# Kernel tuning notes

Hardware: AMD Instinct MI355X
Metric: run time of the kernel (lower is better)

## Reference

```python
import jax, jax.numpy as jnp
import numpy as np

N_NODES = 100000
N_EDGES = 1600000
IN_DIM = 128
HID_DIM = 128
OUT_DIM = 64
BN_EPS = 1e-5


def setup_inputs() -> dict:
    key = jax.random.key(0)
    ks = jax.random.split(key, 8)
    x = jax.random.normal(ks[0], (N_NODES, IN_DIM), dtype=jnp.float32)
    edge_index = jax.random.randint(ks[1], (2, N_EDGES), 0, N_NODES, dtype=jnp.int64)
    s1 = 1.0 / np.sqrt(IN_DIM)
    s2 = 1.0 / np.sqrt(HID_DIM)
    return {
        "x": x,
        "edge_index": edge_index,
        "W1l": jax.random.normal(ks[2], (HID_DIM, IN_DIM), dtype=jnp.float32) * s1,
        "b1l": jnp.zeros((HID_DIM,), dtype=jnp.float32),
        "W1r": jax.random.normal(ks[3], (HID_DIM, IN_DIM), dtype=jnp.float32) * s1,
        "bn_gamma": jnp.ones((HID_DIM,), dtype=jnp.float32),
        "bn_beta": jnp.zeros((HID_DIM,), dtype=jnp.float32),
        "bn_mean": jnp.zeros((HID_DIM,), dtype=jnp.float32),
        "bn_var": jnp.ones((HID_DIM,), dtype=jnp.float32),
        "W2l": jax.random.normal(ks[4], (OUT_DIM, HID_DIM), dtype=jnp.float32) * s2,
        "b2l": jnp.zeros((OUT_DIM,), dtype=jnp.float32),
        "W2r": jax.random.normal(ks[5], (OUT_DIM, HID_DIM), dtype=jnp.float32) * s2,
    }


def _sage_conv(x, src, dst, Wl, bl, Wr, num_nodes):
    # message = x[src], mean-aggregated at dst; out = lin_l(agg) + lin_r(x)
    msgs = x[src]  # [E, D] gather (memory bound)
    agg = jax.ops.segment_sum(msgs, dst, num_segments=num_nodes)
    deg = jax.ops.segment_sum(jnp.ones((src.shape[0],), dtype=x.dtype), dst,
                              num_segments=num_nodes)
    agg = agg / jnp.maximum(deg, 1.0)[:, None]
    return agg @ Wl.T + bl + x @ Wr.T


def reference(x, edge_index, W1l, b1l, W1r, bn_gamma, bn_beta, bn_mean, bn_var,
              W2l, b2l, W2r):
    src, dst = edge_index[0], edge_index[1]
    n = x.shape[0]
    h = _sage_conv(x, src, dst, W1l, b1l, W1r, n)
    # BatchNorm1d (inference: running stats), then ReLU; dropout is identity in eval
    h = (h - bn_mean) * (bn_gamma * jax.lax.rsqrt(bn_var + BN_EPS)) + bn_beta
    h = jax.nn.relu(h)
    return _sage_conv(h, src, dst, W2l, b2l, W2r, n)
```

## Files before the change

kernel.cpp:

```cpp
#include <hip/hip_runtime.h>
#include <hip/hip_fp16.h>

#define N_NODES 100000
#define N_EDGES 1600000
#define TILE 2048
#define NBUK 64
#define BSH 11
#define NBUK_USED ((N_NODES + (1 << BSH) - 1) >> BSH)
#define CAP 36864
#define SMASK 0x1FFFF

typedef _Float16 f16x8 __attribute__((ext_vector_type(8)));
typedef float    f32x4 __attribute__((ext_vector_type(4)));

__global__ __launch_bounds__(256) void k_pre(
    const float* __restrict__ x, __half* __restrict__ x_h,
    const float* __restrict__ W1l, const float* __restrict__ W1r,
    const float* __restrict__ W2l, const float* __restrict__ W2r,
    __half* __restrict__ W1lf, __half* __restrict__ W1rf,
    __half* __restrict__ W2f, int* __restrict__ bcur)
{
    int i = blockIdx.x * 256 + threadIdx.x;
    if (i < N_NODES * 32) {
        float4 v = ((const float4*)x)[i];
        __half2 a = __floats2half2_rn(v.x, v.y);
        __half2 b = __floats2half2_rn(v.z, v.w);
        uint2 u = make_uint2(*(unsigned*)&a, *(unsigned*)&b);
        ((uint2*)x_h)[i] = u;
    }
    if (i < 49152) {
        int tt = i & 16383;
        int j    = tt & 7;
        int lane = (tt >> 3) & 63;
        int ks   = (tt >> 9) & 3;
        int ct   = tt >> 11;
        int m = lane & 15, q = lane >> 4;
        int row = ct * 16 + m;
        int col = ks * 32 + q * 8 + j;
        if (i < 16384) {
            W1lf[tt] = __float2half(W1l[row * 128 + col]);
        } else if (i < 32768) {
            W1rf[tt] = __float2half(W1r[row * 128 + col]);
        } else {
            float v = (ct < 4) ? W2l[row * 128 + col]
                               : W2r[(row - 64) * 128 + col];
            W2f[tt] = __float2half(v);
        }
    }
    if (i < NBUK) bcur[i] = i * CAP;
}

__global__ __launch_bounds__(256) void k_binA(
    const int* __restrict__ ei, int* __restrict__ bcur,
    int2* __restrict__ ebuf)
{
    __shared__ int2 scratch[TILE];
    __shared__ int hist[NBUK];
    __shared__ int tstart[NBUK];
    __shared__ int gbase[NBUK];
    int t = threadIdx.x;
    int e0 = blockIdx.x * TILE;
    int tile_n = min(TILE, N_EDGES - e0);
    if (t < NBUK) hist[t] = 0;
    __syncthreads();
    int srcs[8], dsts[8], rank[8], bks[8];
    #pragma unroll
    for (int i = 0; i < 8; ++i) {
        int e = e0 + i * 256 + t;
        bks[i] = -1;
        if (e < N_EDGES) {
            srcs[i] = ei[e];
            dsts[i] = ei[N_EDGES + e];
            bks[i]  = (dsts[i] >> BSH) & (NBUK - 1);
            rank[i] = atomicAdd(&hist[bks[i]], 1);
        }
    }
    __syncthreads();
    if (t == 0) {
        int s = 0;
        #pragma unroll
        for (int b = 0; b < NBUK; ++b) { tstart[b] = s; s += hist[b]; }
    }
    __syncthreads();
    if (t < NBUK && hist[t] > 0)
        gbase[t] = atomicAdd(&bcur[t], hist[t]);
    __syncthreads();
    #pragma unroll
    for (int i = 0; i < 8; ++i)
        if (bks[i] >= 0) {
            int sl = tstart[bks[i]] + rank[i];
            scratch[min(sl, TILE - 1)] = make_int2(srcs[i], dsts[i]);
        }
    __syncthreads();
    for (int p = t; p < tile_n; p += 256) {
        int2 sd = scratch[p];
        int b = (sd.y >> BSH) & (NBUK - 1);
        int o = gbase[b] + (p - tstart[b]);
        ebuf[min(max(o, 0), NBUK * CAP - 1)] = sd;
    }
}

__global__ __launch_bounds__(1024) void k_fillC2(
    const int2* __restrict__ ebuf, const int* __restrict__ bcur,
    int* __restrict__ row_ptr, int* __restrict__ csr_src)
{
    __shared__ int hist[1 << BSH];
    __shared__ int psum[1024];
    __shared__ int cur[1 << BSH];
    __shared__ int bb_l[NBUK_USED + 1];
    int t = threadIdx.x;
    int b = blockIdx.x;
    int base = b << BSH;
    hist[t] = 0;
    hist[t + 1024] = 0;
    if (t < 64) {
        int c = (t < NBUK_USED) ? (bcur[t] - t * CAP) : 0;
        c = min(max(c, 0), CAP);
        int s = c;
        #pragma unroll
        for (int off = 1; off < 64; off <<= 1) {
            int v = __shfl_up(s, off);
            if (t >= off) s += v;
        }
        if (t < NBUK_USED) bb_l[t] = s - c;
        if (t == NBUK_USED - 1) bb_l[NBUK_USED] = s;
    }
    __syncthreads();
    int bb  = bb_l[b];
    int cnt = min(bb_l[b + 1] - bb, CAP);
    const int2* eb = ebuf + (size_t)b * CAP;
    for (int p = t; p < cnt; p += 1024)
        atomicAdd(&hist[(eb[p].y - base) & ((1 << BSH) - 1)], 1);
    __syncthreads();
    int h0 = hist[2 * t], h1 = hist[2 * t + 1];
    psum[t] = h0 + h1;
    __syncthreads();
    #pragma unroll
    for (int off = 1; off < 1024; off <<= 1) {
        int v = (t >= off) ? psum[t - off] : 0;
        __syncthreads();
        psum[t] += v;
        __syncthreads();
    }
    int e0 = bb + psum[t] - (h0 + h1);
    int e1 = e0 + h0;
    int n0g = base + 2 * t, n1g = n0g + 1;
    if (n0g <= N_NODES) row_ptr[n0g] = e0;
    if (n1g <= N_NODES) row_ptr[n1g] = e1;
    cur[2 * t]     = e0;
    cur[2 * t + 1] = e1;
    __syncthreads();
    for (int p = t; p < cnt; p += 1024) {
        int2 sd = eb[p];
        int pos = atomicAdd(&cur[(sd.y - base) & ((1 << BSH) - 1)], 1);
        csr_src[min(max(pos, 0), N_EDGES - 1)] = sd.x;
    }
}

__device__ __forceinline__ void acc_row8(
    const __half* __restrict__ x_h, int s, int col, float4& acc)
{
    uint2 u = ((const uint2*)(x_h + (size_t)(s & SMASK) * 128))[col];
    __half2 a = *(__half2*)&u.x;
    __half2 b = *(__half2*)&u.y;
    float2 fa = __half22float2(a);
    float2 fb = __half22float2(b);
    acc.x += fa.x; acc.y += fa.y; acc.z += fb.x; acc.w += fb.y;
}

__global__ __launch_bounds__(256) void k_agg1(
    const int* __restrict__ row_ptr, const int* __restrict__ csr_src,
    const __half* __restrict__ x_h, __half* __restrict__ agg_h)
{
    int tid  = threadIdx.x;
    int lane = tid & 63;
    int half = lane >> 5;
    int col  = lane & 31;
    int n    = blockIdx.x * 4 + (tid >> 6);
    int e1 = min(row_ptr[n + 1], N_EDGES);
    int e0 = min(max(row_ptr[n], 0), e1);
    float4 acc = make_float4(0.f, 0.f, 0.f, 0.f);
    for (int eb = e0; eb < e1; eb += 64) {
        int cnt = min(e1 - eb, 64);
        int sv = csr_src[min(eb + lane, N_EDGES - 1)];
        int j = 0;
        for (; j + 8 <= cnt; j += 8) {
            #pragma unroll
            for (int u = 0; u < 4; ++u) {
                int sa = __builtin_amdgcn_readlane(sv, j + 2 * u);
                int sb = __builtin_amdgcn_readlane(sv, j + 2 * u + 1);
                int s  = half ? sb : sa;
                acc_row8(x_h, s, col, acc);
            }
        }
        for (; j + 2 <= cnt; j += 2) {
            int sa = __builtin_amdgcn_readlane(sv, j);
            int sb = __builtin_amdgcn_readlane(sv, j + 1);
            int s  = half ? sb : sa;
            acc_row8(x_h, s, col, acc);
        }
        if (j < cnt) {
            int sa = __builtin_amdgcn_readlane(sv, j);
            if (half == 0) acc_row8(x_h, sa, col, acc);
        }
    }
    acc.x += __shfl_xor(acc.x, 32);
    acc.y += __shfl_xor(acc.y, 32);
    acc.z += __shfl_xor(acc.z, 32);
    acc.w += __shfl_xor(acc.w, 32);
    if (half == 0) {
        __half2 h0 = __floats2half2_rn(acc.x, acc.y);
        __half2 h1 = __floats2half2_rn(acc.z, acc.w);
        uint2 u = make_uint2(*(unsigned*)&h0, *(unsigned*)&h1);
        ((uint2*)agg_h)[n * 32 + col] = u;
    }
}

__global__ __launch_bounds__(256) void k_g12(
    const __half* __restrict__ agg_h, const int* __restrict__ row_ptr,
    const __half* __restrict__ x_h,
    const __half* __restrict__ W1lf, const float* __restrict__ b1l,
    const __half* __restrict__ W1rf,
    const float* __restrict__ gamma, const float* __restrict__ beta,
    const float* __restrict__ mean, const float* __restrict__ var,
    const __half* __restrict__ W2f, const float* __restrict__ b2l,
    __half* __restrict__ p2, float* __restrict__ out)
{
    __shared__ char sm[34816];
    __half (*Aagg)[64][8] = (__half(*)[64][8])sm;
    __half (*Ax)[64][8]   = (__half(*)[64][8])(sm + 16384);
    __half (*Ah)[64][8]   = (__half(*)[64][8])sm;
    float  (*Cs)[132]     = (float(*)[132])sm;
    int tid = threadIdx.x;
    int n0  = blockIdx.x * 64;

    {
        int n  = tid & 63;
        int kg = tid >> 6;
        int ng = n0 + n;
        const uint4* pa = (const uint4*)(agg_h + (size_t)ng * 128 + kg * 32);
        const uint4* px = (const uint4*)(x_h   + (size_t)ng * 128 + kg * 32);
        #pragma unroll
        for (int i = 0; i < 4; ++i) {
            uint4 va = make_uint4(0, 0, 0, 0), vx = va;
            if (ng < N_NODES) { va = pa[i]; vx = px[i]; }
            *(uint4*)&Aagg[kg * 4 + i][n][0] = va;
            *(uint4*)&Ax[kg * 4 + i][n][0]   = vx;
        }
    }
    __syncthreads();

    int lane = tid & 63;
    int w = tid >> 6;
    int m = lane & 15;
    int q = lane >> 4;
    int row = w * 16 + m;
    const __half* bl0 = W1lf + (lane << 3);
    const __half* br0 = W1rf + (lane << 3);
    f32x4 accL[8], accR[8];
    #pragma unroll
    for (int c = 0; c < 8; ++c) {
        accL[c] = (f32x4){0.f, 0.f, 0.f, 0.f};
        accR[c] = (f32x4){0.f, 0.f, 0.f, 0.f};
    }
    #pragma unroll
    for (int ks = 0; ks < 4; ++ks) {
        f16x8 aL = *(const f16x8*)&Aagg[ks * 4 + q][row][0];
        f16x8 aR = *(const f16x8*)&Ax[ks * 4 + q][row][0];
        #pragma unroll
        for (int ct = 0; ct < 8; ++ct) {
            f16x8 bL = *(const f16x8*)(bl0 + ((ct * 4 + ks) << 9));
            f16x8 bR = *(const f16x8*)(br0 + ((ct * 4 + ks) << 9));
            accL[ct] = __builtin_amdgcn_mfma_f32_16x16x32_f16(aL, bL, accL[ct], 0, 0, 0);
            accR[ct] = __builtin_amdgcn_mfma_f32_16x16x32_f16(aR, bR, accR[ct], 0, 0, 0);
        }
    }
    float invd[4];
    #pragma unroll
    for (int r = 0; r < 4; ++r) {
        int n = n0 + w * 16 + q * 4 + r;
        int d = (n < N_NODES) ? (row_ptr[n + 1] - row_ptr[n]) : 1;
        invd[r] = 1.0f / fmaxf((float)d, 1.0f);
    }
    __syncthreads();

    #pragma unroll
    for (int ct = 0; ct < 8; ++ct) {
        int col = ct * 16 + m;
        float s = gamma[col] * rsqrtf(var[col] + 1e-5f);
        float t = beta[col] + (b1l[col] - mean[col]) * s;
        #pragma unroll
        for (int r = 0; r < 4; ++r) {
            float v = accL[ct][r] * invd[r] + accR[ct][r];
            v = fmaxf(v * s + t, 0.f);
            Ah[col >> 3][w * 16 + q * 4 + r][col & 7] = __float2half(v);
        }
    }
    __syncthreads();

    const __half* b0 = W2f + (lane << 3);
    f32x4 acc2[8];
    #pragma unroll
    for (int c = 0; c < 8; ++c) acc2[c] = (f32x4){0.f, 0.f, 0.f, 0.f};
    #pragma unroll
    for (int ks = 0; ks < 4; ++ks) {
        f16x8 a = *(const f16x8*)&Ah[ks * 4 + q][row][0];
        #pragma unroll
        for (int ct = 0; ct < 8; ++ct) {
            f16x8 b = *(const f16x8*)(b0 + ((ct * 4 + ks) << 9));
            acc2[ct] = __builtin_amdgcn_mfma_f32_16x16x32_f16(a, b, acc2[ct], 0, 0, 0);
        }
    }
    __syncthreads();
    #pragma unroll
    for (int ct = 0; ct < 8; ++ct) {
        int col = ct * 16 + m;
        #pragma unroll
        for (int r = 0; r < 4; ++r)
            Cs[w * 16 + q * 4 + r][col] = acc2[ct][r];
    }
    __syncthreads();
    {
        int rr = tid & 63;
        int pg = tid >> 6;
        int ng = n0 + rr;
        if (ng < N_NODES) {
            union { __half hh[16]; uint4 u[2]; } tmp;
            #pragma unroll
            for (int c = 0; c < 16; ++c)
                tmp.hh[c] = __float2half(Cs[rr][pg * 16 + c]);
            uint4* dp = (uint4*)(p2 + (size_t)ng * 64 + pg * 16);
            dp[0] = tmp.u[0];
            dp[1] = tmp.u[1];
            #pragma unroll
            for (int i = 0; i < 4; ++i) {
                float4 v  = *(const float4*)&Cs[rr][64 + pg * 16 + i * 4];
                float4 bb = *(const float4*)(b2l + pg * 16 + i * 4);
                v.x += bb.x; v.y += bb.y; v.z += bb.z; v.w += bb.w;
                *(float4*)(out + (size_t)ng * 64 + pg * 16 + i * 4) = v;
            }
        }
    }
}

__device__ __forceinline__ void acc_row_p2(
    const __half* __restrict__ p2, int s, int lane, float4& acc)
{
    uint2 u = ((const uint2*)(p2 + (size_t)(s & SMASK) * 64))[lane];
    __half2 a = *(__half2*)&u.x;
    __half2 b = *(__half2*)&u.y;
    float2 fa = __half22float2(a);
    float2 fb = __half22float2(b);
    acc.x += fa.x; acc.y += fa.y; acc.z += fb.x; acc.w += fb.y;
}

__global__ __launch_bounds__(256) void k_agg2(
    const int* __restrict__ row_ptr, const int* __restrict__ csr_src,
    const __half* __restrict__ p2, float* __restrict__ out)
{
    int tid  = threadIdx.x;
    int n    = blockIdx.x * 16 + (tid >> 4);
    int lane = tid & 15;
    int e1 = min(row_ptr[n + 1], N_EDGES);
    int e0 = min(max(row_ptr[n], 0), e1);
    float4 acc = make_float4(0.f, 0.f, 0.f, 0.f);
    int e = e0;
    for (; e + 4 <= e1; e += 4) {
        int s0 = csr_src[e], s1 = csr_src[e + 1];
        int s2 = csr_src[e + 2], s3 = csr_src[e + 3];
        acc_row_p2(p2, s0, lane, acc);
        acc_row_p2(p2, s1, lane, acc);
        acc_row_p2(p2, s2, lane, acc);
        acc_row_p2(p2, s3, lane, acc);
    }
    for (; e < e1; ++e) acc_row_p2(p2, csr_src[e], lane, acc);
    float inv = 1.0f / fmaxf((float)(e1 - e0), 1.0f);
    float4* o = (float4*)out + n * 16 + lane;
    float4 cur = *o;
    cur.x += acc.x * inv; cur.y += acc.y * inv;
    cur.z += acc.z * inv; cur.w += acc.w * inv;
    *o = cur;
}

extern "C" void kernel_launch(void* const* d_in, const int* in_sizes, int n_in,
                              void* d_out, int out_size, void* d_ws, size_t ws_size,
                              hipStream_t stream)
{
    const float* x     = (const float*)d_in[0];
    const int*   ei    = (const int*)d_in[1];
    const float* W1l   = (const float*)d_in[2];
    const float* b1l   = (const float*)d_in[3];
    const float* W1r   = (const float*)d_in[4];
    const float* gamma = (const float*)d_in[5];
    const float* beta  = (const float*)d_in[6];
    const float* mean  = (const float*)d_in[7];
    const float* var   = (const float*)d_in[8];
    const float* W2l   = (const float*)d_in[9];
    const float* b2l   = (const float*)d_in[10];
    const float* W2r   = (const float*)d_in[11];
    float* out = (float*)d_out;

    char* ws = (char*)d_ws;
    __half* agg_h   = (__half*)(ws);
    __half* p2      = (__half*)(ws + 25600000);
    __half* x_h     = (__half*)(ws + 51200000);
    int*    csr_src = (int*)(ws + 76800000);
    int*    row_ptr = (int*)(ws + 83200000);
    __half* W1lf    = (__half*)(ws + 83600016);
    __half* W1rf    = (__half*)(ws + 83632784);
    __half* W2f     = (__half*)(ws + 83665552);
    int2*   ebuf    = (int2*)(ws + 83698320);
    int*    bcur    = (int*)(ws + 102572688);

    k_pre<<<12500, 256, 0, stream>>>(x, x_h, W1l, W1r, W2l, W2r,
                                     W1lf, W1rf, W2f, bcur);
    k_binA<<<(N_EDGES + TILE - 1) / TILE, 256, 0, stream>>>(ei, bcur, ebuf);
    k_fillC2<<<NBUK_USED, 1024, 0, stream>>>(ebuf, bcur, row_ptr, csr_src);
    k_agg1<<<N_NODES / 4, 256, 0, stream>>>(row_ptr, csr_src, x_h, agg_h);
    k_g12<<<(N_NODES + 63) / 64, 256, 0, stream>>>(agg_h, row_ptr, x_h,
                                                   W1lf, b1l, W1rf,
                                                   gamma, beta, mean, var,
                                                   W2f, b2l, p2, out);
    k_agg2<<<N_NODES / 16, 256, 0, stream>>>(row_ptr, csr_src, p2, out);
}
```

Before: 327.7 us.

## Fuse preprocessing with edge binning and load GEMM operands directly to registers

The x/weight fp16 conversion kernel and the edge-binning kernel become one launch, with blocks split by index, and bucket counters are zeroed by a memset and stored as relative offsets. In the fused GEMM kernel, A operands are loaded straight from global memory into registers instead of being staged through LDS, and the LDS staging of the second GEMM's output is removed in favour of direct scalar stores. This cuts a launch and several barriers and LDS round trips. The cost is narrower global stores for p2 and out (2- and 4-byte per lane instead of 16-byte vectors) and less coalesced A loads.

```diff
diff --git a/kernel.cpp b/kernel.cpp
--- a/kernel.cpp
+++ b/kernel.cpp
@@ -9,48 +9,18 @@
 #define NBUK_USED ((N_NODES + (1 << BSH) - 1) >> BSH)
 #define CAP 36864
 #define SMASK 0x1FFFF
+#define PRE_BLOCKS 12500
+#define BINA_BLOCKS ((N_EDGES + TILE - 1) / TILE)
 
 typedef _Float16 f16x8 __attribute__((ext_vector_type(8)));
 typedef float    f32x4 __attribute__((ext_vector_type(4)));
 
-__global__ __launch_bounds__(256) void k_pre(
+__global__ __launch_bounds__(256) void k_preA(
     const float* __restrict__ x, __half* __restrict__ x_h,
     const float* __restrict__ W1l, const float* __restrict__ W1r,
     const float* __restrict__ W2l, const float* __restrict__ W2r,
     __half* __restrict__ W1lf, __half* __restrict__ W1rf,
-    __half* __restrict__ W2f, int* __restrict__ bcur)
-{
-    int i = blockIdx.x * 256 + threadIdx.x;
-    if (i < N_NODES * 32) {
-        float4 v = ((const float4*)x)[i];
-        __half2 a = __floats2half2_rn(v.x, v.y);
-        __half2 b = __floats2half2_rn(v.z, v.w);
-        uint2 u = make_uint2(*(unsigned*)&a, *(unsigned*)&b);
-        ((uint2*)x_h)[i] = u;
-    }
-    if (i < 49152) {
-        int tt = i & 16383;
-        int j    = tt & 7;
-        int lane = (tt >> 3) & 63;
-        int ks   = (tt >> 9) & 3;
-        int ct   = tt >> 11;
-        int m = lane & 15, q = lane >> 4;
-        int row = ct * 16 + m;
-        int col = ks * 32 + q * 8 + j;
-        if (i < 16384) {
-            W1lf[tt] = __float2half(W1l[row * 128 + col]);
-        } else if (i < 32768) {
-            W1rf[tt] = __float2half(W1r[row * 128 + col]);
-        } else {
-            float v = (ct < 4) ? W2l[row * 128 + col]
-                               : W2r[(row - 64) * 128 + col];
-            W2f[tt] = __float2half(v);
-        }
-    }
-    if (i < NBUK) bcur[i] = i * CAP;
-}
-
-__global__ __launch_bounds__(256) void k_binA(
+    __half* __restrict__ W2f,
     const int* __restrict__ ei, int* __restrict__ bcur,
     int2* __restrict__ ebuf)
 {
@@ -59,7 +29,39 @@
     __shared__ int tstart[NBUK];
     __shared__ int gbase[NBUK];
     int t = threadIdx.x;
-    int e0 = blockIdx.x * TILE;
+
+    if (blockIdx.x < PRE_BLOCKS) {
+        int i = blockIdx.x * 256 + t;
+        if (i < N_NODES * 32) {
+            float4 v = ((const float4*)x)[i];
+            __half2 a = __floats2half2_rn(v.x, v.y);
+            __half2 b = __floats2half2_rn(v.z, v.w);
+            uint2 u = make_uint2(*(unsigned*)&a, *(unsigned*)&b);
+            ((uint2*)x_h)[i] = u;
+        }
+        if (i < 49152) {
+            int tt = i & 16383;
+            int j    = tt & 7;
+            int lane = (tt >> 3) & 63;
+            int ks   = (tt >> 9) & 3;
+            int ct   = tt >> 11;
+            int m = lane & 15, q = lane >> 4;
+            int row = ct * 16 + m;
+            int col = ks * 32 + q * 8 + j;
+            if (i < 16384) {
+                W1lf[tt] = __float2half(W1l[row * 128 + col]);
+            } else if (i < 32768) {
+                W1rf[tt] = __float2half(W1r[row * 128 + col]);
+            } else {
+                float v = (ct < 4) ? W2l[row * 128 + col]
+                                   : W2r[(row - 64) * 128 + col];
+                W2f[tt] = __float2half(v);
+            }
+        }
+        return;
+    }
+
+    int e0 = (blockIdx.x - PRE_BLOCKS) * TILE;
     int tile_n = min(TILE, N_EDGES - e0);
     if (t < NBUK) hist[t] = 0;
     __syncthreads();
@@ -83,7 +85,7 @@
     }
     __syncthreads();
     if (t < NBUK && hist[t] > 0)
-        gbase[t] = atomicAdd(&bcur[t], hist[t]);
+        gbase[t] = t * CAP + atomicAdd(&bcur[t], hist[t]);
     __syncthreads();
     #pragma unroll
     for (int i = 0; i < 8; ++i)
@@ -114,7 +116,7 @@
     hist[t] = 0;
     hist[t + 1024] = 0;
     if (t < 64) {
-        int c = (t < NBUK_USED) ? (bcur[t] - t * CAP) : 0;
+        int c = (t < NBUK_USED) ? bcur[t] : 0;
         c = min(max(c, 0), CAP);
         int s = c;
         #pragma unroll
@@ -226,35 +228,30 @@
     const __half* __restrict__ W2f, const float* __restrict__ b2l,
     __half* __restrict__ p2, float* __restrict__ out)
 {
-    __shared__ char sm[34816];
-    __half (*Aagg)[64][8] = (__half(*)[64][8])sm;
-    __half (*Ax)[64][8]   = (__half(*)[64][8])(sm + 16384);
-    __half (*Ah)[64][8]   = (__half(*)[64][8])sm;
-    float  (*Cs)[132]     = (float(*)[132])sm;
-    int tid = threadIdx.x;
-    int n0  = blockIdx.x * 64;
-
-    {
-        int n  = tid & 63;
-        int kg = tid >> 6;
-        int ng = n0 + n;
-        const uint4* pa = (const uint4*)(agg_h + (size_t)ng * 128 + kg * 32);
-        const uint4* px = (const uint4*)(x_h   + (size_t)ng * 128 + kg * 32);
-        #pragma unroll
-        for (int i = 0; i < 4; ++i) {
-            uint4 va = make_uint4(0, 0, 0, 0), vx = va;
-            if (ng < N_NODES) { va = pa[i]; vx = px[i]; }
-            *(uint4*)&Aagg[kg * 4 + i][n][0] = va;
-            *(uint4*)&Ax[kg * 4 + i][n][0]   = vx;
-        }
-    }
-    __syncthreads();
-
+    __shared__ __half Ah[16][64][8];
+    int tid  = threadIdx.x;
     int lane = tid & 63;
-    int w = tid >> 6;
-    int m = lane & 15;
-    int q = lane >> 4;
-    int row = w * 16 + m;
+    int w    = tid >> 6;
+    int m    = lane & 15;
+    int q    = lane >> 4;
+    int n0   = blockIdx.x * 64;
+
+    int arow = n0 + w * 16 + m;
+    bool aok = arow < N_NODES;
+    const __half* pa = agg_h + (size_t)(aok ? arow : 0) * 128 + q * 8;
+    const __half* px = x_h   + (size_t)(aok ? arow : 0) * 128 + q * 8;
+    f16x8 aL[4], aR[4];
+    #pragma unroll
+    for (int ks = 0; ks < 4; ++ks) {
+        f16x8 va = {}, vx = {};
+        if (aok) {
+            va = *(const f16x8*)(pa + ks * 32);
+            vx = *(const f16x8*)(px + ks * 32);
+        }
+        aL[ks] = va;
+        aR[ks] = vx;
+    }
+
     const __half* bl0 = W1lf + (lane << 3);
     const __half* br0 = W1rf + (lane << 3);
     f32x4 accL[8], accR[8];
@@ -265,14 +262,12 @@
     }
     #pragma unroll
     for (int ks = 0; ks < 4; ++ks) {
-        f16x8 aL = *(const f16x8*)&Aagg[ks * 4 + q][row][0];
-        f16x8 aR = *(const f16x8*)&Ax[ks * 4 + q][row][0];
         #pragma unroll
         for (int ct = 0; ct < 8; ++ct) {
             f16x8 bL = *(const f16x8*)(bl0 + ((ct * 4 + ks) << 9));
             f16x8 bR = *(const f16x8*)(br0 + ((ct * 4 + ks) << 9));
-            accL[ct] = __builtin_amdgcn_mfma_f32_16x16x32_f16(aL, bL, accL[ct], 0, 0, 0);
-            accR[ct] = __builtin_amdgcn_mfma_f32_16x16x32_f16(aR, bR, accR[ct], 0, 0, 0);
+            accL[ct] = __builtin_amdgcn_mfma_f32_16x16x32_f16(aL[ks], bL, accL[ct], 0, 0, 0);
+            accR[ct] = __builtin_amdgcn_mfma_f32_16x16x32_f16(aR[ks], bR, accR[ct], 0, 0, 0);
         }
     }
     float invd[4];
@@ -282,7 +277,6 @@
         int d = (n < N_NODES) ? (row_ptr[n + 1] - row_ptr[n]) : 1;
         invd[r] = 1.0f / fmaxf((float)d, 1.0f);
     }
-    __syncthreads();
 
     #pragma unroll
     for (int ct = 0; ct < 8; ++ct) {
@@ -304,40 +298,25 @@
     for (int c = 0; c < 8; ++c) acc2[c] = (f32x4){0.f, 0.f, 0.f, 0.f};
     #pragma unroll
     for (int ks = 0; ks < 4; ++ks) {
-        f16x8 a = *(const f16x8*)&Ah[ks * 4 + q][row][0];
+        f16x8 a = *(const f16x8*)&Ah[ks * 4 + q][w * 16 + m][0];
         #pragma unroll
         for (int ct = 0; ct < 8; ++ct) {
             f16x8 b = *(const f16x8*)(b0 + ((ct * 4 + ks) << 9));
             acc2[ct] = __builtin_amdgcn_mfma_f32_16x16x32_f16(a, b, acc2[ct], 0, 0, 0);
         }
     }
-    __syncthreads();
-    #pragma unroll
-    for (int ct = 0; ct < 8; ++ct) {
-        int col = ct * 16 + m;
-        #pragma unroll
-        for (int r = 0; r < 4; ++r)
-            Cs[w * 16 + q * 4 + r][col] = acc2[ct][r];
-    }
-    __syncthreads();
-    {
-        int rr = tid & 63;
-        int pg = tid >> 6;
-        int ng = n0 + rr;
+
+    #pragma unroll
+    for (int r = 0; r < 4; ++r) {
+        int ng = n0 + w * 16 + q * 4 + r;
         if (ng < N_NODES) {
-            union { __half hh[16]; uint4 u[2]; } tmp;
             #pragma unroll
-            for (int c = 0; c < 16; ++c)
-                tmp.hh[c] = __float2half(Cs[rr][pg * 16 + c]);
-            uint4* dp = (uint4*)(p2 + (size_t)ng * 64 + pg * 16);
-            dp[0] = tmp.u[0];
-            dp[1] = tmp.u[1];
+            for (int ct = 0; ct < 4; ++ct)
+                p2[(size_t)ng * 64 + ct * 16 + m] = __float2half(acc2[ct][r]);
             #pragma unroll
-            for (int i = 0; i < 4; ++i) {
-                float4 v  = *(const float4*)&Cs[rr][64 + pg * 16 + i * 4];
-                float4 bb = *(const float4*)(b2l + pg * 16 + i * 4);
-                v.x += bb.x; v.y += bb.y; v.z += bb.z; v.w += bb.w;
-                *(float4*)(out + (size_t)ng * 64 + pg * 16 + i * 4) = v;
+            for (int ct = 4; ct < 8; ++ct) {
+                int c = (ct - 4) * 16 + m;
+                out[(size_t)ng * 64 + c] = acc2[ct][r] + b2l[c];
             }
         }
     }
@@ -412,9 +391,9 @@
     int2*   ebuf    = (int2*)(ws + 83698320);
     int*    bcur    = (int*)(ws + 102572688);
 
-    k_pre<<<12500, 256, 0, stream>>>(x, x_h, W1l, W1r, W2l, W2r,
-                                     W1lf, W1rf, W2f, bcur);
-    k_binA<<<(N_EDGES + TILE - 1) / TILE, 256, 0, stream>>>(ei, bcur, ebuf);
+    hipMemsetAsync(bcur, 0, NBUK * sizeof(int), stream);
+    k_preA<<<PRE_BLOCKS + BINA_BLOCKS, 256, 0, stream>>>(
+        x, x_h, W1l, W1r, W2l, W2r, W1lf, W1rf, W2f, ei, bcur, ebuf);
     k_fillC2<<<NBUK_USED, 1024, 0, stream>>>(ebuf, bcur, row_ptr, csr_src);
     k_agg1<<<N_NODES / 4, 256, 0, stream>>>(row_ptr, csr_src, x_h, agg_h);
     k_g12<<<(N_NODES + 63) / 64, 256, 0, stream>>>(agg_h, row_ptr, x_h,
```

Measured after the change: 310.0 us. -5.4%, faster.
